# Kernel tuning notes

Measured on AMD Instinct MI355X. Metric: run time of the kernel, lower is better.

The kernel has to match this reference:

```python
import jax, jax.numpy as jnp
import numpy as np

B, T, C = 8, 2048, 1024
HEAD = 64


def setup_inputs() -> dict:
    key = jax.random.key(0)
    kx, kk, kq, kv = jax.random.split(key, 4)
    scale = 1.0 / np.sqrt(C)
    x = jax.random.normal(kx, (B, T, C), dtype=jnp.float32)
    # nn.Linear(n_embd, head_size, bias=False) weight shape: (head_size, n_embd)
    Wk = jax.random.normal(kk, (HEAD, C), dtype=jnp.float32) * scale
    Wq = jax.random.normal(kq, (HEAD, C), dtype=jnp.float32) * scale
    Wv = jax.random.normal(kv, (HEAD, C), dtype=jnp.float32) * scale
    return {"x": x, "Wk": Wk, "Wq": Wq, "Wv": Wv}


def reference(x, Wk, Wq, Wv):
    Bb, Tt, Cc = x.shape
    k = jnp.einsum('btc,hc->bth', x, Wk)  # (B,T,head)
    q = jnp.einsum('btc,hc->bth', x, Wq)
    v = jnp.einsum('btc,hc->bth', x, Wv)
    scaling = Cc ** (-0.5)  # NOTE: scales by full embed dim C, per source
    wei = jnp.einsum('bth,bsh->bts', q, k) * scaling  # (B,T,T)
    causal = jnp.tril(jnp.ones((Tt, Tt), dtype=bool))
    wei = jnp.where(causal, wei, -jnp.inf)
    wei = jax.nn.softmax(wei, axis=-1)  # stable max-subtract softmax (= _safe_softmax)
    out = jnp.einsum('bts,bsh->bth', wei, v)  # (B,T,head)
    return out
```

## Files before the change

kernel.cpp:

```cpp
#include <hip/hip_runtime.h>
#include <math.h>

#define B_ 8
#define T_ 2048
#define C_ 1024
#define H_ 64
#define M_ (B_ * T_)

typedef short bf8 __attribute__((ext_vector_type(8)));
typedef float f32x4 __attribute__((ext_vector_type(4)));

__device__ __forceinline__ unsigned short f2b(float f) {
    unsigned u = __float_as_uint(f);
    u += 0x7fffu + ((u >> 16) & 1u);
    return (unsigned short)(u >> 16);
}
__device__ __forceinline__ float b2f(unsigned short u) {
    return __uint_as_float(((unsigned)u) << 16);
}
__device__ __forceinline__ unsigned pack2(float lo, float hi) {
    unsigned a = __float_as_uint(lo) + 0x8000u;
    unsigned b = __float_as_uint(hi) + 0x8000u;
    return __builtin_amdgcn_perm(b, a, 0x07060302u);
}

__global__ __launch_bounds__(256) void wconv_kernel(
    const float* __restrict__ Wk, const float* __restrict__ Wq,
    const float* __restrict__ Wv, unsigned short* __restrict__ Wb)
{
    int idx = (blockIdx.x * 256 + threadIdx.x) * 4;
    int n = idx >> 10;
    int c = idx & 1023;
    const float* src = (n < 64)  ? (Wq + (size_t)n * C_ + c)
                     : (n < 128) ? (Wk + (size_t)(n - 64) * C_ + c)
                                 : (Wv + (size_t)(n - 128) * C_ + c);
    float4 v = *(const float4*)src;
    *(ushort4*)(Wb + idx) = make_ushort4(f2b(v.x), f2b(v.y), f2b(v.z), f2b(v.w));
}

__global__ __launch_bounds__(256) void qkv_kernel(
    const float* __restrict__ x, const unsigned short* __restrict__ Wb,
    unsigned short* __restrict__ qo, unsigned short* __restrict__ kP,
    unsigned short* __restrict__ vP)
{
    __shared__ unsigned short As[2][64 * 64];
    __shared__ unsigned short Bs[2][96 * 64];

    const int tid  = threadIdx.x;
    const int lane = tid & 63;
    const int w    = tid >> 6;
    const int m15  = lane & 15;
    const int q4   = lane >> 4;
    const int wr   = w >> 1;
    const int wc   = w & 1;
    const int r0   = blockIdx.x * 64;
    const int c0   = blockIdx.y * 96;

    const int arow = tid >> 2;
    const int acq  = tid & 3;
    const float* xp = x + (size_t)(r0 + arow) * C_ + acq * 16;
    const int aw0 = arow * 64 + (((acq * 2)     ^ (arow & 7)) * 8);
    const int aw1 = arow * 64 + (((acq * 2 + 1) ^ (arow & 7)) * 8);

    int brow[3], bch[3];
#pragma unroll
    for (int s = 0; s < 3; ++s) {
        int flat = tid + 256 * s;
        brow[s] = flat >> 3;
        bch[s]  = flat & 7;
    }

    f32x4 acc[2][3];
#pragma unroll
    for (int i = 0; i < 2; ++i)
#pragma unroll
        for (int j = 0; j < 3; ++j) acc[i][j] = f32x4{0.f, 0.f, 0.f, 0.f};

    float4 xa[4];
    bf8 wreg[3];
#pragma unroll
    for (int qq = 0; qq < 4; ++qq) xa[qq] = *(const float4*)(xp + 4 * qq);
#pragma unroll
    for (int s = 0; s < 3; ++s)
        wreg[s] = *(const bf8*)(Wb + (size_t)(c0 + brow[s]) * C_ + bch[s] * 8);

    {
        uint4 u0 = {pack2(xa[0].x, xa[0].y), pack2(xa[0].z, xa[0].w),
                    pack2(xa[1].x, xa[1].y), pack2(xa[1].z, xa[1].w)};
        uint4 u1 = {pack2(xa[2].x, xa[2].y), pack2(xa[2].z, xa[2].w),
                    pack2(xa[3].x, xa[3].y), pack2(xa[3].z, xa[3].w)};
        *(uint4*)&As[0][aw0] = u0;
        *(uint4*)&As[0][aw1] = u1;
#pragma unroll
        for (int s = 0; s < 3; ++s)
            *(bf8*)&Bs[0][brow[s] * 64 + ((bch[s] ^ (brow[s] & 7)) * 8)] = wreg[s];
    }

    const int swzbase = m15 & 7;
    for (int ck = 0; ck < 16; ++ck) {
        const int nxt = ck + 1;
        if (nxt < 16) {
            const int k0 = nxt * 64;
#pragma unroll
            for (int qq = 0; qq < 4; ++qq) xa[qq] = *(const float4*)(xp + k0 + 4 * qq);
#pragma unroll
            for (int s = 0; s < 3; ++s)
                wreg[s] = *(const bf8*)(Wb + (size_t)(c0 + brow[s]) * C_ + k0 + bch[s] * 8);
        }
        __syncthreads();
        const int buf = ck & 1;
#pragma unroll
        for (int kc = 0; kc < 2; ++kc) {
            const int swz = ((4 * kc + q4) ^ swzbase) * 8;
            bf8 af[2], bfr[3];
#pragma unroll
            for (int i = 0; i < 2; ++i)
                af[i] = *(const bf8*)&As[buf][(32 * wr + 16 * i + m15) * 64 + swz];
#pragma unroll
            for (int j = 0; j < 3; ++j)
                bfr[j] = *(const bf8*)&Bs[buf][(48 * wc + 16 * j + m15) * 64 + swz];
#pragma unroll
            for (int i = 0; i < 2; ++i)
#pragma unroll
                for (int j = 0; j < 3; ++j)
                    acc[i][j] = __builtin_amdgcn_mfma_f32_16x16x32_bf16(
                        af[i], bfr[j], acc[i][j], 0, 0, 0);
        }
        if (nxt < 16) {
            const int nb = nxt & 1;
            uint4 u0 = {pack2(xa[0].x, xa[0].y), pack2(xa[0].z, xa[0].w),
                        pack2(xa[1].x, xa[1].y), pack2(xa[1].z, xa[1].w)};
            uint4 u1 = {pack2(xa[2].x, xa[2].y), pack2(xa[2].z, xa[2].w),
                        pack2(xa[3].x, xa[3].y), pack2(xa[3].z, xa[3].w)};
            *(uint4*)&As[nb][aw0] = u0;
            *(uint4*)&As[nb][aw1] = u1;
#pragma unroll
            for (int s = 0; s < 3; ++s)
                *(bf8*)&Bs[nb][brow[s] * 64 + ((bch[s] ^ (brow[s] & 7)) * 8)] = wreg[s];
        }
    }

#pragma unroll
    for (int i = 0; i < 2; ++i) {
#pragma unroll
        for (int j = 0; j < 3; ++j) {
            const int base = c0 + 48 * wc + 16 * j;
            if (base < 64) {
#pragma unroll
                for (int r = 0; r < 4; ++r) {
                    int t = r0 + 32 * wr + 16 * i + 4 * q4 + r;
                    qo[(size_t)t * H_ + base + m15] = f2b(acc[i][j][r]);
                }
            } else if (base < 128) {
                const int D0 = base - 64;
                const int f  = D0 >> 5;
                const int c1 = (D0 >> 3) & 3;
                const int l2 = (c1 + (m15 >> 3)) * 16;
#pragma unroll
                for (int r = 0; r < 4; ++r) {
                    int t  = r0 + 32 * wr + 16 * i + 4 * q4 + r;
                    int bb = t >> 11, tt = t & 2047;
                    kP[(size_t)bb * 131072 +
                       (size_t)((((tt >> 4) * 2 + f) * 64 + l2 + (tt & 15)) * 8 + (m15 & 7))]
                        = f2b(acc[i][j][r]);
                }
            } else {
                const int cg = (base - 128) >> 4;
#pragma unroll
                for (int r = 0; r < 4; ++r) {
                    int t  = r0 + 32 * wr + 16 * i + 4 * q4 + r;
                    int bb = t >> 11, tt = t & 2047;
                    int lv = ((tt & 31) >> 3) * 16 + m15;
                    vP[(size_t)bb * 131072 +
                       (size_t)((((tt >> 5) * 4 + cg) * 64 + lv) * 8 + (tt & 7))]
                        = f2b(acc[i][j][r]);
                }
            }
        }
    }
}

__global__ __launch_bounds__(512) void attn_kernel(
    const unsigned short* __restrict__ qo, const unsigned short* __restrict__ kP,
    const unsigned short* __restrict__ vP, float* __restrict__ outp)
{
    __shared__ unsigned short Pl[8][2][16 * 40];
    __shared__ float Al[8][2][16];
    __shared__ float Ml[2][4][2][2][16];
    __shared__ unsigned short Ob[2][3][2][16 * 64];

    const int tid  = threadIdx.x;
    const int lane = tid & 63;
    const int w    = tid >> 6;
    const int m15  = lane & 15;
    const int q4   = lane >> 4;
    const int b    = blockIdx.x;
    const int y    = blockIdx.y;
    const int gsel = w >> 2;
    const int s    = w & 3;
    const int g    = gsel ? (63 - y) : y;
    const int trow = 32 * g;

    const unsigned short* qb = qo + (size_t)b * T_ * H_;
    const unsigned short* kb = kP + (size_t)b * 131072;
    const unsigned short* vb = vP + (size_t)b * 131072;

    bf8 qf[2][2];
#pragma unroll
    for (int gq = 0; gq < 2; ++gq)
#pragma unroll
        for (int f = 0; f < 2; ++f)
            qf[gq][f] = *(const bf8*)(qb + (size_t)(trow + 16 * gq + m15) * H_ + 32 * f + 8 * q4);

    f32x4 o[2][4];
#pragma unroll
    for (int gq = 0; gq < 2; ++gq)
#pragma unroll
        for (int cg = 0; cg < 4; ++cg) o[gq][cg] = f32x4{0.f, 0.f, 0.f, 0.f};
    float mr[2] = {-INFINITY, -INFINITY};
    float lr[2] = {0.f, 0.f};

    bf8 kf[2][2], vf[4];
    if (s <= g) {
#pragma unroll
        for (int t2 = 0; t2 < 2; ++t2)
#pragma unroll
            for (int f = 0; f < 2; ++f)
                kf[t2][f] = *(const bf8*)(kb + (size_t)(((2 * s + t2) * 2 + f) * 64 + lane) * 8);
#pragma unroll
        for (int cg = 0; cg < 4; ++cg)
            vf[cg] = *(const bf8*)(vb + (size_t)((s * 4 + cg) * 64 + lane) * 8);
    }

    for (int kt = s; kt <= g; kt += 4) {
        const bool more = (kt + 4 <= g);
        bf8 kn[2][2], vn[4];
        if (more) {
            const int t16 = 2 * (kt + 4);
#pragma unroll
            for (int t2 = 0; t2 < 2; ++t2)
#pragma unroll
                for (int f = 0; f < 2; ++f)
                    kn[t2][f] = *(const bf8*)(kb + (size_t)(((t16 + t2) * 2 + f) * 64 + lane) * 8);
#pragma unroll
            for (int cg = 0; cg < 4; ++cg)
                vn[cg] = *(const bf8*)(vb + (size_t)(((kt + 4) * 4 + cg) * 64 + lane) * 8);
        }

#pragma unroll
        for (int gq = 0; gq < 2; ++gq) {
            f32x4 sa[2];
            sa[0] = f32x4{0.f, 0.f, 0.f, 0.f};
            sa[1] = f32x4{0.f, 0.f, 0.f, 0.f};
#pragma unroll
            for (int t2 = 0; t2 < 2; ++t2)
#pragma unroll
                for (int f = 0; f < 2; ++f)
                    sa[t2] = __builtin_amdgcn_mfma_f32_16x16x32_bf16(
                        kf[t2][f], qf[gq][f], sa[t2], 0, 0, 0);

            float sc[2][4];
#pragma unroll
            for (int t2 = 0; t2 < 2; ++t2)
#pragma unroll
                for (int r = 0; r < 4; ++r)
                    sc[t2][r] = sa[t2][r] * 0.03125f;

            if (kt == g) {
#pragma unroll
                for (int t2 = 0; t2 < 2; ++t2)
#pragma unroll
                    for (int r = 0; r < 4; ++r)
                        if (32 * kt + 16 * t2 + 4 * q4 + r > trow + 16 * gq + m15)
                            sc[t2][r] = -INFINITY;
            }

            float vm = fmaxf(fmaxf(fmaxf(sc[0][0], sc[0][1]), fmaxf(sc[0][2], sc[0][3])),
                             fmaxf(fmaxf(sc[1][0], sc[1][1]), fmaxf(sc[1][2], sc[1][3])));
            vm = fmaxf(vm, __shfl_xor(vm, 16));
            vm = fmaxf(vm, __shfl_xor(vm, 32));
            float mn = fmaxf(mr[gq], vm);
            float al = __expf(mr[gq] - mn);
            float sum = 0.f;
#pragma unroll
            for (int t2 = 0; t2 < 2; ++t2)
#pragma unroll
                for (int r = 0; r < 4; ++r) {
                    sc[t2][r] = __expf(sc[t2][r] - mn);
                    sum += sc[t2][r];
                }
            sum += __shfl_xor(sum, 16);
            sum += __shfl_xor(sum, 32);
            lr[gq] = lr[gq] * al + sum;
            mr[gq] = mn;

#pragma unroll
            for (int t2 = 0; t2 < 2; ++t2) {
                ushort4 pk = make_ushort4(f2b(sc[t2][0]), f2b(sc[t2][1]),
                                          f2b(sc[t2][2]), f2b(sc[t2][3]));
                *(ushort4*)&Pl[w][gq][m15 * 40 + 16 * t2 + 4 * q4] = pk;
            }
            if (q4 == 0) Al[w][gq][m15] = al;
            bf8 pf   = *(const bf8*)&Pl[w][gq][m15 * 40 + q4 * 8];
            f32x4 av = *(const f32x4*)&Al[w][gq][q4 * 4];

#pragma unroll
            for (int cg = 0; cg < 4; ++cg) {
#pragma unroll
                for (int r = 0; r < 4; ++r) o[gq][cg][r] *= av[r];
                o[gq][cg] = __builtin_amdgcn_mfma_f32_16x16x32_bf16(
                    pf, vf[cg], o[gq][cg], 0, 0, 0);
            }
        }

        if (more) {
#pragma unroll
            for (int t2 = 0; t2 < 2; ++t2)
#pragma unroll
                for (int f = 0; f < 2; ++f) kf[t2][f] = kn[t2][f];
#pragma unroll
            for (int cg = 0; cg < 4; ++cg) vf[cg] = vn[cg];
        }
    }

    if (q4 == 0) {
#pragma unroll
        for (int gq = 0; gq < 2; ++gq) {
            Ml[gsel][s][gq][0][m15] = mr[gq];
            Ml[gsel][s][gq][1][m15] = lr[gq];
        }
    }
    if (s >= 1) {
#pragma unroll
        for (int gq = 0; gq < 2; ++gq)
#pragma unroll
            for (int cg = 0; cg < 4; ++cg)
#pragma unroll
                for (int r = 0; r < 4; ++r)
                    Ob[gsel][s - 1][gq][(4 * q4 + r) * 64 + 16 * cg + m15] = f2b(o[gq][cg][r]);
    }
    __syncthreads();
    if (s == 0) {
        float* op = outp + (size_t)(b * T_ + trow) * H_;
#pragma unroll
        for (int gq = 0; gq < 2; ++gq) {
#pragma unroll
            for (int r = 0; r < 4; ++r) {
                const int qq = 4 * q4 + r;
                float mi[4], li[4];
#pragma unroll
                for (int i = 0; i < 4; ++i) {
                    mi[i] = Ml[gsel][i][gq][0][qq];
                    li[i] = Ml[gsel][i][gq][1][qq];
                }
                float M = fmaxf(fmaxf(mi[0], mi[1]), fmaxf(mi[2], mi[3]));
                float wt[4];
                float L = 0.f;
#pragma unroll
                for (int i = 0; i < 4; ++i) { wt[i] = __expf(mi[i] - M); L += li[i] * wt[i]; }
                float inv = 1.0f / L;
#pragma unroll
                for (int cg = 0; cg < 4; ++cg) {
                    float a = o[gq][cg][r] * wt[0];
#pragma unroll
                    for (int i = 1; i < 4; ++i)
                        a += b2f(Ob[gsel][i - 1][gq][qq * 64 + 16 * cg + m15]) * wt[i];
                    op[(size_t)(16 * gq + qq) * H_ + 16 * cg + m15] = a * inv;
                }
            }
        }
    }
}

extern "C" void kernel_launch(void* const* d_in, const int* in_sizes, int n_in,
                              void* d_out, int out_size, void* d_ws, size_t ws_size,
                              hipStream_t stream) {
    const float* x  = (const float*)d_in[0];
    const float* Wk = (const float*)d_in[1];
    const float* Wq = (const float*)d_in[2];
    const float* Wv = (const float*)d_in[3];
    char* ws = (char*)d_ws;
    unsigned short* Wb = (unsigned short*)ws;
    unsigned short* qo = (unsigned short*)(ws + 0x080000);
    unsigned short* kP = (unsigned short*)(ws + 0x280000);
    unsigned short* vP = (unsigned short*)(ws + 0x480000);

    wconv_kernel<<<192, 256, 0, stream>>>(Wk, Wq, Wv, Wb);
    qkv_kernel<<<dim3(M_ / 64, 2), 256, 0, stream>>>(x, Wb, qo, kP, vP);
    attn_kernel<<<dim3(8, 32), 512, 0, stream>>>(qo, kP, vP, (float*)d_out);
}
```

Measured before the change: 136.2 us.

## Widen QKV GEMM to all 192 columns and use 64-key attention tiles

The QKV projection kernel now computes all 192 output columns (q,k,v) per block instead of splitting them across two blocks along y. Each x tile is then loaded and converted to bf16 once rather than twice, at the cost of more accumulator registers and twice the shared memory for the weight tile. The attention kernel processes 64 keys per iteration instead of 32, using a swizzled P buffer and two PV MFMAs per column group. This halves the number of online-softmax rescale and reduction steps, but V is no longer prefetched one iteration ahead, and the causal tail wastes more work when the tile extends past the diagonal.

```diff
diff --git a/kernel.cpp b/kernel.cpp
--- a/kernel.cpp
+++ b/kernel.cpp
@@ -44,7 +44,7 @@
     unsigned short* __restrict__ vP)
 {
     __shared__ unsigned short As[2][64 * 64];
-    __shared__ unsigned short Bs[2][96 * 64];
+    __shared__ unsigned short Bs[2][192 * 64];
 
     const int tid  = threadIdx.x;
     const int lane = tid & 63;
@@ -54,7 +54,6 @@
     const int wr   = w >> 1;
     const int wc   = w & 1;
     const int r0   = blockIdx.x * 64;
-    const int c0   = blockIdx.y * 96;
 
     const int arow = tid >> 2;
     const int acq  = tid & 3;
@@ -62,27 +61,27 @@
     const int aw0 = arow * 64 + (((acq * 2)     ^ (arow & 7)) * 8);
     const int aw1 = arow * 64 + (((acq * 2 + 1) ^ (arow & 7)) * 8);
 
-    int brow[3], bch[3];
-#pragma unroll
-    for (int s = 0; s < 3; ++s) {
+    int brow[6], bch[6];
+#pragma unroll
+    for (int s = 0; s < 6; ++s) {
         int flat = tid + 256 * s;
         brow[s] = flat >> 3;
         bch[s]  = flat & 7;
     }
 
-    f32x4 acc[2][3];
+    f32x4 acc[2][6];
 #pragma unroll
     for (int i = 0; i < 2; ++i)
 #pragma unroll
-        for (int j = 0; j < 3; ++j) acc[i][j] = f32x4{0.f, 0.f, 0.f, 0.f};
+        for (int j = 0; j < 6; ++j) acc[i][j] = f32x4{0.f, 0.f, 0.f, 0.f};
 
     float4 xa[4];
-    bf8 wreg[3];
+    bf8 wreg[6];
 #pragma unroll
     for (int qq = 0; qq < 4; ++qq) xa[qq] = *(const float4*)(xp + 4 * qq);
 #pragma unroll
-    for (int s = 0; s < 3; ++s)
-        wreg[s] = *(const bf8*)(Wb + (size_t)(c0 + brow[s]) * C_ + bch[s] * 8);
+    for (int s = 0; s < 6; ++s)
+        wreg[s] = *(const bf8*)(Wb + (size_t)brow[s] * C_ + bch[s] * 8);
 
     {
         uint4 u0 = {pack2(xa[0].x, xa[0].y), pack2(xa[0].z, xa[0].w),
@@ -92,7 +91,7 @@
         *(uint4*)&As[0][aw0] = u0;
         *(uint4*)&As[0][aw1] = u1;
 #pragma unroll
-        for (int s = 0; s < 3; ++s)
+        for (int s = 0; s < 6; ++s)
             *(bf8*)&Bs[0][brow[s] * 64 + ((bch[s] ^ (brow[s] & 7)) * 8)] = wreg[s];
     }
 
@@ -104,25 +103,25 @@
 #pragma unroll
             for (int qq = 0; qq < 4; ++qq) xa[qq] = *(const float4*)(xp + k0 + 4 * qq);
 #pragma unroll
-            for (int s = 0; s < 3; ++s)
-                wreg[s] = *(const bf8*)(Wb + (size_t)(c0 + brow[s]) * C_ + k0 + bch[s] * 8);
+            for (int s = 0; s < 6; ++s)
+                wreg[s] = *(const bf8*)(Wb + (size_t)brow[s] * C_ + k0 + bch[s] * 8);
         }
         __syncthreads();
         const int buf = ck & 1;
 #pragma unroll
         for (int kc = 0; kc < 2; ++kc) {
             const int swz = ((4 * kc + q4) ^ swzbase) * 8;
-            bf8 af[2], bfr[3];
+            bf8 af[2], bfr[6];
 #pragma unroll
             for (int i = 0; i < 2; ++i)
                 af[i] = *(const bf8*)&As[buf][(32 * wr + 16 * i + m15) * 64 + swz];
 #pragma unroll
-            for (int j = 0; j < 3; ++j)
-                bfr[j] = *(const bf8*)&Bs[buf][(48 * wc + 16 * j + m15) * 64 + swz];
+            for (int j = 0; j < 6; ++j)
+                bfr[j] = *(const bf8*)&Bs[buf][(96 * wc + 16 * j + m15) * 64 + swz];
 #pragma unroll
             for (int i = 0; i < 2; ++i)
 #pragma unroll
-                for (int j = 0; j < 3; ++j)
+                for (int j = 0; j < 6; ++j)
                     acc[i][j] = __builtin_amdgcn_mfma_f32_16x16x32_bf16(
                         af[i], bfr[j], acc[i][j], 0, 0, 0);
         }
@@ -135,7 +134,7 @@
             *(uint4*)&As[nb][aw0] = u0;
             *(uint4*)&As[nb][aw1] = u1;
 #pragma unroll
-            for (int s = 0; s < 3; ++s)
+            for (int s = 0; s < 6; ++s)
                 *(bf8*)&Bs[nb][brow[s] * 64 + ((bch[s] ^ (brow[s] & 7)) * 8)] = wreg[s];
         }
     }
@@ -143,8 +142,8 @@
 #pragma unroll
     for (int i = 0; i < 2; ++i) {
 #pragma unroll
-        for (int j = 0; j < 3; ++j) {
-            const int base = c0 + 48 * wc + 16 * j;
+        for (int j = 0; j < 6; ++j) {
+            const int base = 96 * wc + 16 * j;
             if (base < 64) {
 #pragma unroll
                 for (int r = 0; r < 4; ++r) {
@@ -184,7 +183,7 @@
     const unsigned short* __restrict__ qo, const unsigned short* __restrict__ kP,
     const unsigned short* __restrict__ vP, float* __restrict__ outp)
 {
-    __shared__ unsigned short Pl[8][2][16 * 40];
+    __shared__ unsigned short Pl[8][2][16 * 64];
     __shared__ float Al[8][2][16];
     __shared__ float Ml[2][4][2][2][16];
     __shared__ unsigned short Ob[2][3][2][16 * 64];
@@ -200,6 +199,7 @@
     const int s    = w & 3;
     const int g    = gsel ? (63 - y) : y;
     const int trow = 32 * g;
+    const int last = g >> 1;
 
     const unsigned short* qb = qo + (size_t)b * T_ * H_;
     const unsigned short* kb = kP + (size_t)b * 131072;
@@ -220,70 +220,73 @@
     float mr[2] = {-INFINITY, -INFINITY};
     float lr[2] = {0.f, 0.f};
 
-    bf8 kf[2][2], vf[4];
-    if (s <= g) {
-#pragma unroll
-        for (int t2 = 0; t2 < 2; ++t2)
+    bf8 kf[4][2];
+    if (s <= last) {
+#pragma unroll
+        for (int t2 = 0; t2 < 4; ++t2)
 #pragma unroll
             for (int f = 0; f < 2; ++f)
-                kf[t2][f] = *(const bf8*)(kb + (size_t)(((2 * s + t2) * 2 + f) * 64 + lane) * 8);
-#pragma unroll
-        for (int cg = 0; cg < 4; ++cg)
-            vf[cg] = *(const bf8*)(vb + (size_t)((s * 4 + cg) * 64 + lane) * 8);
-    }
-
-    for (int kt = s; kt <= g; kt += 4) {
-        const bool more = (kt + 4 <= g);
-        bf8 kn[2][2], vn[4];
+                kf[t2][f] = *(const bf8*)(kb + (size_t)(((4 * s + t2) * 2 + f) * 64 + lane) * 8);
+    }
+
+    const int swz = m15 & 7;
+    for (int kt = s; kt <= last; kt += 4) {
+        const bool more = (kt + 4 <= last);
+        bf8 kn[4][2];
         if (more) {
-            const int t16 = 2 * (kt + 4);
-#pragma unroll
-            for (int t2 = 0; t2 < 2; ++t2)
+#pragma unroll
+            for (int t2 = 0; t2 < 4; ++t2)
 #pragma unroll
                 for (int f = 0; f < 2; ++f)
-                    kn[t2][f] = *(const bf8*)(kb + (size_t)(((t16 + t2) * 2 + f) * 64 + lane) * 8);
+                    kn[t2][f] = *(const bf8*)(kb + (size_t)(((4 * (kt + 4) + t2) * 2 + f) * 64 + lane) * 8);
+        }
+        bf8 vf[2][4];
+#pragma unroll
+        for (int kc = 0; kc < 2; ++kc)
 #pragma unroll
             for (int cg = 0; cg < 4; ++cg)
-                vn[cg] = *(const bf8*)(vb + (size_t)(((kt + 4) * 4 + cg) * 64 + lane) * 8);
-        }
+                vf[kc][cg] = *(const bf8*)(vb + (size_t)(((2 * kt + kc) * 4 + cg) * 64 + lane) * 8);
 
 #pragma unroll
         for (int gq = 0; gq < 2; ++gq) {
-            f32x4 sa[2];
-            sa[0] = f32x4{0.f, 0.f, 0.f, 0.f};
-            sa[1] = f32x4{0.f, 0.f, 0.f, 0.f};
-#pragma unroll
-            for (int t2 = 0; t2 < 2; ++t2)
+            f32x4 sa[4];
+#pragma unroll
+            for (int t2 = 0; t2 < 4; ++t2) sa[t2] = f32x4{0.f, 0.f, 0.f, 0.f};
+#pragma unroll
+            for (int t2 = 0; t2 < 4; ++t2)
 #pragma unroll
                 for (int f = 0; f < 2; ++f)
                     sa[t2] = __builtin_amdgcn_mfma_f32_16x16x32_bf16(
                         kf[t2][f], qf[gq][f], sa[t2], 0, 0, 0);
 
-            float sc[2][4];
-#pragma unroll
-            for (int t2 = 0; t2 < 2; ++t2)
+            float sc[4][4];
+#pragma unroll
+            for (int t2 = 0; t2 < 4; ++t2)
 #pragma unroll
                 for (int r = 0; r < 4; ++r)
                     sc[t2][r] = sa[t2][r] * 0.03125f;
 
-            if (kt == g) {
-#pragma unroll
-                for (int t2 = 0; t2 < 2; ++t2)
+            if (kt == last) {
+#pragma unroll
+                for (int t2 = 0; t2 < 4; ++t2)
 #pragma unroll
                     for (int r = 0; r < 4; ++r)
-                        if (32 * kt + 16 * t2 + 4 * q4 + r > trow + 16 * gq + m15)
+                        if (64 * kt + 16 * t2 + 4 * q4 + r > trow + 16 * gq + m15)
                             sc[t2][r] = -INFINITY;
             }
 
-            float vm = fmaxf(fmaxf(fmaxf(sc[0][0], sc[0][1]), fmaxf(sc[0][2], sc[0][3])),
-                             fmaxf(fmaxf(sc[1][0], sc[1][1]), fmaxf(sc[1][2], sc[1][3])));
+            float vm = -INFINITY;
+#pragma unroll
+            for (int t2 = 0; t2 < 4; ++t2)
+#pragma unroll
+                for (int r = 0; r < 4; ++r) vm = fmaxf(vm, sc[t2][r]);
             vm = fmaxf(vm, __shfl_xor(vm, 16));
             vm = fmaxf(vm, __shfl_xor(vm, 32));
             float mn = fmaxf(mr[gq], vm);
             float al = __expf(mr[gq] - mn);
             float sum = 0.f;
 #pragma unroll
-            for (int t2 = 0; t2 < 2; ++t2)
+            for (int t2 = 0; t2 < 4; ++t2)
 #pragma unroll
                 for (int r = 0; r < 4; ++r) {
                     sc[t2][r] = __expf(sc[t2][r] - mn);
@@ -295,13 +298,17 @@
             mr[gq] = mn;
 
 #pragma unroll
-            for (int t2 = 0; t2 < 2; ++t2) {
+            for (int t2 = 0; t2 < 4; ++t2) {
                 ushort4 pk = make_ushort4(f2b(sc[t2][0]), f2b(sc[t2][1]),
                                           f2b(sc[t2][2]), f2b(sc[t2][3]));
-                *(ushort4*)&Pl[w][gq][m15 * 40 + 16 * t2 + 4 * q4] = pk;
+                int c = 2 * t2 + (q4 >> 1);
+                *(ushort4*)&Pl[w][gq][m15 * 64 + ((c ^ swz) * 8) + (q4 & 1) * 4] = pk;
             }
             if (q4 == 0) Al[w][gq][m15] = al;
-            bf8 pf   = *(const bf8*)&Pl[w][gq][m15 * 40 + q4 * 8];
+            bf8 pf[2];
+#pragma unroll
+            for (int kc = 0; kc < 2; ++kc)
+                pf[kc] = *(const bf8*)&Pl[w][gq][m15 * 64 + (((4 * kc + q4) ^ swz) * 8)];
             f32x4 av = *(const f32x4*)&Al[w][gq][q4 * 4];
 
 #pragma unroll
@@ -309,17 +316,17 @@
 #pragma unroll
                 for (int r = 0; r < 4; ++r) o[gq][cg][r] *= av[r];
                 o[gq][cg] = __builtin_amdgcn_mfma_f32_16x16x32_bf16(
-                    pf, vf[cg], o[gq][cg], 0, 0, 0);
+                    pf[0], vf[0][cg], o[gq][cg], 0, 0, 0);
+                o[gq][cg] = __builtin_amdgcn_mfma_f32_16x16x32_bf16(
+                    pf[1], vf[1][cg], o[gq][cg], 0, 0, 0);
             }
         }
 
         if (more) {
 #pragma unroll
-            for (int t2 = 0; t2 < 2; ++t2)
+            for (int t2 = 0; t2 < 4; ++t2)
 #pragma unroll
                 for (int f = 0; f < 2; ++f) kf[t2][f] = kn[t2][f];
-#pragma unroll
-            for (int cg = 0; cg < 4; ++cg) vf[cg] = vn[cg];
         }
     }
 
@@ -386,6 +393,6 @@
     unsigned short* vP = (unsigned short*)(ws + 0x480000);
 
     wconv_kernel<<<192, 256, 0, stream>>>(Wk, Wq, Wv, Wb);
-    qkv_kernel<<<dim3(M_ / 64, 2), 256, 0, stream>>>(x, Wb, qo, kP, vP);
+    qkv_kernel<<<M_ / 64, 256, 0, stream>>>(x, Wb, qo, kP, vP);
     attn_kernel<<<dim3(8, 32), 512, 0, stream>>>(qo, kP, vP, (float*)d_out);
 }
```

After: 128.8 us. 5.5% less time.
